# Optimization experiments

Hardware: AMD Instinct MI355X
Metric: run time of the kernel (lower is better)

## Reference

```python
import jax, jax.numpy as jnp
import numpy as np

D_MODEL = 1024
N_HEADS = 16
HEAD_DIM = D_MODEL // N_HEADS
BATCH = 4
SEQ = 2048
NEG_INF = -1000000000.0  # matches torch masked_fill value in source


def setup_inputs() -> dict:
    key = jax.random.key(0)
    ks = jax.random.split(key, 5)
    scale = 1.0 / np.sqrt(D_MODEL)
    x = jax.random.normal(ks[0], (BATCH, SEQ, D_MODEL), dtype=jnp.float32)
    wq = jax.random.normal(ks[1], (D_MODEL, D_MODEL), dtype=jnp.float32) * scale
    wk = jax.random.normal(ks[2], (D_MODEL, D_MODEL), dtype=jnp.float32) * scale
    wv = jax.random.normal(ks[3], (D_MODEL, D_MODEL), dtype=jnp.float32) * scale
    wo = jax.random.normal(ks[4], (D_MODEL, D_MODEL), dtype=jnp.float32) * scale
    return {"x": x, "wq": wq, "wk": wk, "wv": wv, "wo": wo}


def reference(x, wq, wk, wv, wo):
    b, s, d = x.shape
    # projections (weights applied as x @ W^T, matching nn-style Linear weights)
    q = jnp.einsum('bsd,ed->bse', x, wq).reshape(b, s, N_HEADS, HEAD_DIM).transpose(0, 2, 1, 3)
    k = jnp.einsum('bsd,ed->bse', x, wk).reshape(b, s, N_HEADS, HEAD_DIM).transpose(0, 2, 1, 3)
    v = jnp.einsum('bsd,ed->bse', x, wv).reshape(b, s, N_HEADS, HEAD_DIM).transpose(0, 2, 1, 3)
    # scaled dot-product scores [b, h, s, s]
    scores = jnp.einsum('bhqd,bhkd->bhqk', q, k) / jnp.sqrt(jnp.float32(HEAD_DIM))
    # causal mask: positions strictly above diagonal masked with -1e9
    causal = jnp.triu(jnp.ones((s, s), dtype=bool), k=1)
    scores = jnp.where(causal[None, None], jnp.float32(NEG_INF), scores)
    attn = jax.nn.softmax(scores, axis=-1)
    out = jnp.einsum('bhqk,bhkd->bhqd', attn, v)
    out = out.transpose(0, 2, 1, 3).reshape(b, s, d)
    return jnp.einsum('bsd,ed->bse', out, wo)
```

## Files before the change

kernel.cpp:

```cpp
#include <hip/hip_runtime.h>
#include <hip/hip_bf16.h>

typedef __hip_bfloat16 bf16;
typedef __attribute__((ext_vector_type(8))) short short8;
typedef __attribute__((ext_vector_type(4))) short short4_t;
typedef __attribute__((ext_vector_type(4))) float f32x4;
typedef unsigned int u32;

#define MFMA16(a, b, c) __builtin_amdgcn_mfma_f32_16x16x32_bf16(a, b, c, 0, 0, 0)

#if __has_builtin(__builtin_amdgcn_exp2f)
#define EXP2(x) __builtin_amdgcn_exp2f(x)
#else
#define EXP2(x) __expf((x) * 0.6931471805599453f)
#endif

static constexpr int S_ = 2048, D_ = 1024, M_ = 8192;
static constexpr size_t SZ = (size_t)M_ * D_;
static constexpr size_t WSZ = (size_t)D_ * D_;
static constexpr float QSCALE = 0.125f * 1.4426950408889634f;

__device__ __forceinline__ void gload16(void* lds, const void* g) {
  __builtin_amdgcn_global_load_lds((const __attribute__((address_space(1))) void*)g,
                                   (__attribute__((address_space(3))) void*)lds, 16, 0, 0);
}

__device__ __forceinline__ short4_t cvt4(const float4 v) {
  short4_t r;
  r[0] = (short)__bfloat16_as_ushort(__float2bfloat16(v.x));
  r[1] = (short)__bfloat16_as_ushort(__float2bfloat16(v.y));
  r[2] = (short)__bfloat16_as_ushort(__float2bfloat16(v.z));
  r[3] = (short)__bfloat16_as_ushort(__float2bfloat16(v.w));
  return r;
}

__device__ __forceinline__ u32 pk2(float a, float b) {
  return (u32)__bfloat16_as_ushort(__float2bfloat16(a)) |
         ((u32)__bfloat16_as_ushort(__float2bfloat16(b)) << 16);
}

__global__ __launch_bounds__(256) void cvt_f32_bf16(const float* __restrict__ in,
                                                    bf16* __restrict__ out, int n4) {
  int stride = gridDim.x * 256;
  for (int i = blockIdx.x * 256 + threadIdx.x; i < n4; i += stride) {
    float4 v = ((const float4*)in)[i];
    *(short4_t*)&out[(size_t)i * 4] = cvt4(v);
  }
}

__global__ __launch_bounds__(256) void cvt_all(const float* __restrict__ x,
                                               const float* __restrict__ wq,
                                               const float* __restrict__ wk,
                                               const float* __restrict__ wv,
                                               const float* __restrict__ wo,
                                               bf16* __restrict__ xb,
                                               bf16* __restrict__ wqkv,
                                               bf16* __restrict__ wob, int nseg) {
  const int X4 = (int)(SZ / 4);
  const int per = 1 << 18;
  int total = X4 + nseg * per;
  for (int i = blockIdx.x * 256 + threadIdx.x; i < total; i += gridDim.x * 256) {
    const float* s;
    bf16* d;
    int off;
    if (i < X4) {
      s = x; d = xb; off = i;
    } else {
      int j = i - X4;
      int seg = j >> 18;
      off = j & (per - 1);
      s = (seg == 0) ? wq : (seg == 1) ? wk : (seg == 2) ? wv : wo;
      d = (seg < 3) ? (wqkv + ((size_t)seg << 20)) : wob;
    }
    float4 v = ((const float4*)s)[off];
    *(short4_t*)&d[(size_t)off * 4] = cvt4(v);
  }
}

#define GSTAGE(buf, kt)                                                              \
  {                                                                                  \
    _Pragma("unroll") for (int i_ = 0; i_ < 2; ++i_) {                               \
      int c_ = i_ * 256 + tid;                                                       \
      int row_ = c_ >> 2, col_ = (c_ & 3) * 8;                                       \
      gload16(&lA[buf][c_ * 8], &A[(size_t)(m0 + row_) * 1024 + (kt) * 32 + col_]);  \
      gload16(&lB[buf][c_ * 8], &W[(size_t)(n0 + row_) * 1024 + (kt) * 32 + col_]);  \
    }                                                                                \
  }

__global__ __launch_bounds__(256) void qkv_gemm(const bf16* __restrict__ A,
                                                const bf16* __restrict__ Wqkv,
                                                bf16* __restrict__ QKV) {
  __shared__ __align__(16) bf16 lA[2][128 * 32];
  __shared__ __align__(16) bf16 lB[2][128 * 32];
  const int tid = threadIdx.x, lane = tid & 63, w = tid >> 6;
  const int wr = w >> 1, wc = w & 1;
  const int m0 = blockIdx.x * 128;
  const int mat = blockIdx.y >> 3, n0 = (blockIdx.y & 7) * 128;
  const bf16* W = Wqkv + (size_t)mat * WSZ;
  bf16* C = QKV + (size_t)mat * SZ;
  const int l15 = lane & 15, lg = lane >> 4;

  f32x4 zero = {0.f, 0.f, 0.f, 0.f};
  f32x4 acc[4][4];
#pragma unroll
  for (int i = 0; i < 4; i++)
#pragma unroll
    for (int j = 0; j < 4; j++) acc[i][j] = zero;

  GSTAGE(0, 0);
  int cur = 0;
  for (int kt = 0; kt < 32; ++kt) {
    if (kt + 1 < 32) {
      GSTAGE(cur ^ 1, kt + 1);
      asm volatile("s_waitcnt vmcnt(4)" ::: "memory");
    } else {
      asm volatile("s_waitcnt vmcnt(0)" ::: "memory");
    }
    __builtin_amdgcn_s_barrier();

    short8 af[4], bfr[4];
#pragma unroll
    for (int mi = 0; mi < 4; mi++)
      af[mi] = *(const short8*)&lA[cur][(wr * 64 + mi * 16 + l15) * 32 + lg * 8];
#pragma unroll
    for (int ni = 0; ni < 4; ni++)
      bfr[ni] = *(const short8*)&lB[cur][(wc * 64 + ni * 16 + l15) * 32 + lg * 8];
    if (mat == 2) {
#pragma unroll
      for (int mi = 0; mi < 4; mi++)
#pragma unroll
        for (int ni = 0; ni < 4; ni++) acc[mi][ni] = MFMA16(af[mi], bfr[ni], acc[mi][ni]);
    } else {
#pragma unroll
      for (int mi = 0; mi < 4; mi++)
#pragma unroll
        for (int ni = 0; ni < 4; ni++) acc[mi][ni] = MFMA16(bfr[ni], af[mi], acc[mi][ni]);
    }
    __builtin_amdgcn_s_barrier();
    cur ^= 1;
  }

  if (mat == 2) {
#pragma unroll
    for (int mi = 0; mi < 4; mi++)
#pragma unroll
      for (int ni = 0; ni < 4; ni++) {
        int mB = m0 + wr * 64 + mi * 16 + lg * 4;
        int n = n0 + wc * 64 + ni * 16 + l15;
        int b = mB >> 11, s = mB & 2047, h = n >> 6, dh = n & 63;
        uint2 dd = {pk2(acc[mi][ni][0], acc[mi][ni][1]),
                    pk2(acc[mi][ni][2], acc[mi][ni][3])};
        *(uint2*)&C[((size_t)((b << 4) + h) * 64 + dh) * 2048 + s] = dd;
      }
  } else {
    const float scale = (mat == 0) ? QSCALE : 1.0f;
#pragma unroll
    for (int mi = 0; mi < 4; mi++)
#pragma unroll
      for (int ni = 0; ni < 4; ni++) {
        int m = m0 + wr * 64 + mi * 16 + l15;
        int nB = n0 + wc * 64 + ni * 16 + lg * 4;
        int b = m >> 11, s = m & 2047, h = nB >> 6, dh = nB & 63;
        uint2 dd = {pk2(acc[mi][ni][0] * scale, acc[mi][ni][1] * scale),
                    pk2(acc[mi][ni][2] * scale, acc[mi][ni][3] * scale)};
        *(uint2*)&C[((size_t)((b << 4) + h) * 2048 + s) * 64 + dh] = dd;
      }
  }
}

__global__ __launch_bounds__(256) void gemm_out(const bf16* __restrict__ A,
                                                const bf16* __restrict__ W,
                                                float* __restrict__ C) {
  __shared__ __align__(16) bf16 lA[2][128 * 32];
  __shared__ __align__(16) bf16 lB[2][128 * 32];
  const int tid = threadIdx.x, lane = tid & 63, w = tid >> 6;
  const int wr = w >> 1, wc = w & 1;
  const int m0 = blockIdx.x * 128, n0 = blockIdx.y * 128;
  const int l15 = lane & 15, lg = lane >> 4;

  f32x4 zero = {0.f, 0.f, 0.f, 0.f};
  f32x4 acc[4][4];
#pragma unroll
  for (int i = 0; i < 4; i++)
#pragma unroll
    for (int j = 0; j < 4; j++) acc[i][j] = zero;

  GSTAGE(0, 0);
  int cur = 0;
  for (int kt = 0; kt < 32; ++kt) {
    if (kt + 1 < 32) {
      GSTAGE(cur ^ 1, kt + 1);
      asm volatile("s_waitcnt vmcnt(4)" ::: "memory");
    } else {
      asm volatile("s_waitcnt vmcnt(0)" ::: "memory");
    }
    __builtin_amdgcn_s_barrier();

    short8 af[4], bfr[4];
#pragma unroll
    for (int mi = 0; mi < 4; mi++)
      af[mi] = *(const short8*)&lA[cur][(wr * 64 + mi * 16 + l15) * 32 + lg * 8];
#pragma unroll
    for (int ni = 0; ni < 4; ni++)
      bfr[ni] = *(const short8*)&lB[cur][(wc * 64 + ni * 16 + l15) * 32 + lg * 8];
#pragma unroll
    for (int mi = 0; mi < 4; mi++)
#pragma unroll
      for (int ni = 0; ni < 4; ni++) acc[mi][ni] = MFMA16(bfr[ni], af[mi], acc[mi][ni]);
    __builtin_amdgcn_s_barrier();
    cur ^= 1;
  }

#pragma unroll
  for (int mi = 0; mi < 4; mi++)
#pragma unroll
    for (int ni = 0; ni < 4; ni++) {
      int m = m0 + wr * 64 + mi * 16 + l15;
      int nB = n0 + wc * 64 + ni * 16 + lg * 4;
      float4 v = {acc[mi][ni][0], acc[mi][ni][1], acc[mi][ni][2], acc[mi][ni][3]};
      *(float4*)&C[(size_t)m * 1024 + nB] = v;
    }
}

__global__ __launch_bounds__(256, 3) void attn_fwd(const bf16* __restrict__ Q,
                                                   const bf16* __restrict__ K,
                                                   const bf16* __restrict__ Vt,
                                                   bf16* __restrict__ O) {
  __shared__ __align__(16) bf16 lK[2][64 * 64];
  __shared__ __align__(16) bf16 lV[2][64 * 64];
  __shared__ __align__(16) bf16 lP[4][32 * 64];
  const int tid = threadIdx.x, lane = tid & 63, w = tid >> 6;
  const int l15 = lane & 15, lg = lane >> 4;
  const int bh = blockIdx.x;
  const int qb = 15 - blockIdx.y;
  const int q0 = qb * 128 + w * 32;
  const bf16* Qb = Q + (size_t)bh * S_ * 64;
  const bf16* Kb = K + (size_t)bh * S_ * 64;
  const bf16* Vb = Vt + (size_t)bh * 64 * S_;
  bf16* Pw = lP[w];

  short8 qf[2][2];
#pragma unroll
  for (int mi = 0; mi < 2; mi++)
#pragma unroll
    for (int kd = 0; kd < 2; kd++)
      qf[mi][kd] = *(const short8*)&Qb[(size_t)(q0 + mi * 16 + l15) * 64 + kd * 32 + lg * 8];

  f32x4 zero = {0.f, 0.f, 0.f, 0.f};
  f32x4 acc[2][4];
  float mr[2], lr[2];
#pragma unroll
  for (int mi = 0; mi < 2; mi++) {
    mr[mi] = -1e9f;
    lr[mi] = 0.f;
#pragma unroll
    for (int ni = 0; ni < 4; ni++) acc[mi][ni] = zero;
  }

  const int nch = (qb + 1) * 2;

#define STAGE(buf, c)                                                                   \
  {                                                                                     \
    _Pragma("unroll") for (int i = 0; i < 2; ++i) {                                     \
      int t2 = i * 256 + tid;                                                           \
      int row = t2 >> 3;                                                                \
      int cb = ((t2 & 7) * 16) ^ ((row & 7) << 4);                                      \
      gload16((char*)lK[buf] + t2 * 16, (const char*)Kb + (size_t)((c) * 64 + row) * 128 + cb); \
      gload16((char*)lV[buf] + t2 * 16, (const char*)Vb + (size_t)row * 4096 + (size_t)(c) * 128 + cb); \
    }                                                                                   \
  }

  STAGE(0, 0);
  int cur = 0;
  for (int c = 0; c < nch; ++c) {
    __builtin_amdgcn_s_barrier();
    if (c + 1 < nch) {
      STAGE(cur ^ 1, c + 1);
      asm volatile("s_waitcnt vmcnt(4)" ::: "memory");
    } else {
      asm volatile("s_waitcnt vmcnt(0)" ::: "memory");
    }
    __builtin_amdgcn_s_barrier();

    if (c * 64 <= q0 + 31) {
      const int c0 = c * 64;
      f32x4 sc[2][4];
#pragma unroll
      for (int mi = 0; mi < 2; mi++)
#pragma unroll
        for (int ch = 0; ch < 4; ch++) sc[mi][ch] = zero;
      const char* Kc = (const char*)lK[cur];
      __builtin_amdgcn_s_setprio(1);
#pragma unroll
      for (int kd = 0; kd < 2; ++kd)
#pragma unroll
        for (int ch = 0; ch < 4; ++ch) {
          short8 kf = *(const short8*)(Kc + (ch * 16 + l15) * 128 + ((kd * 64 + lg * 16) ^ ((l15 & 7) << 4)));
          sc[0][ch] = MFMA16(kf, qf[0][kd], sc[0][ch]);
          sc[1][ch] = MFMA16(kf, qf[1][kd], sc[1][ch]);
        }
      __builtin_amdgcn_s_setprio(0);

      if (c0 + 63 > q0) {
#pragma unroll
        for (int mi = 0; mi < 2; mi++) {
          int q = q0 + mi * 16 + l15;
#pragma unroll
          for (int ch = 0; ch < 4; ch++)
#pragma unroll
            for (int r = 0; r < 4; r++) {
              int kv = c0 + ch * 16 + lg * 4 + r;
              if (kv > q) sc[mi][ch][r] = -1e9f;
            }
        }
      }

#pragma unroll
      for (int mi = 0; mi < 2; mi++) {
        float v0 = fmaxf(fmaxf(sc[mi][0][0], sc[mi][0][1]), fmaxf(sc[mi][0][2], sc[mi][0][3]));
        float v1 = fmaxf(fmaxf(sc[mi][1][0], sc[mi][1][1]), fmaxf(sc[mi][1][2], sc[mi][1][3]));
        float v2 = fmaxf(fmaxf(sc[mi][2][0], sc[mi][2][1]), fmaxf(sc[mi][2][2], sc[mi][2][3]));
        float v3 = fmaxf(fmaxf(sc[mi][3][0], sc[mi][3][1]), fmaxf(sc[mi][3][2], sc[mi][3][3]));
        float vmax = fmaxf(fmaxf(v0, v1), fmaxf(v2, v3));
        vmax = fmaxf(vmax, __shfl_xor(vmax, 16));
        vmax = fmaxf(vmax, __shfl_xor(vmax, 32));
        if (!__all(vmax <= mr[mi] + 8.f)) {
          float mn = fmaxf(mr[mi], vmax);
          float corr = EXP2(mr[mi] - mn);
          mr[mi] = mn;
          lr[mi] *= corr;
#pragma unroll
          for (int r = 0; r < 4; r++) {
            float cr = __shfl(corr, (lane & 48) | (((lane >> 4) << 2) + r));
#pragma unroll
            for (int ni = 0; ni < 4; ni++) acc[mi][ni][r] *= cr;
          }
        }
        float ps0 = 0.f, ps1 = 0.f, ps2 = 0.f, ps3 = 0.f;
#pragma unroll
        for (int ch = 0; ch < 4; ch++) {
          float p0 = EXP2(sc[mi][ch][0] - mr[mi]);
          float p1 = EXP2(sc[mi][ch][1] - mr[mi]);
          float p2 = EXP2(sc[mi][ch][2] - mr[mi]);
          float p3 = EXP2(sc[mi][ch][3] - mr[mi]);
          sc[mi][ch][0] = p0; sc[mi][ch][1] = p1; sc[mi][ch][2] = p2; sc[mi][ch][3] = p3;
          ps0 += p0; ps1 += p1; ps2 += p2; ps3 += p3;
        }
        float ps = (ps0 + ps1) + (ps2 + ps3);
        ps += __shfl_xor(ps, 16);
        ps += __shfl_xor(ps, 32);
        lr[mi] += ps;
        int row = mi * 16 + l15;
        char* Pb = (char*)Pw + row * 128;
        int sw = (row & 7) << 4;
#pragma unroll
        for (int ch = 0; ch < 4; ch++) {
          u32 d0 = pk2(sc[mi][ch][0], sc[mi][ch][1]);
          u32 d1 = pk2(sc[mi][ch][2], sc[mi][ch][3]);
          uint2 dd = {d0, d1};
          *(uint2*)(Pb + ((ch * 32 + lg * 8) ^ sw)) = dd;
        }
      }

      asm volatile("s_waitcnt lgkmcnt(0)" ::: "memory");
      const char* Vc = (const char*)lV[cur];
      __builtin_amdgcn_s_setprio(1);
#pragma unroll
      for (int kd = 0; kd < 2; ++kd) {
        short8 pf[2];
#pragma unroll
        for (int mi = 0; mi < 2; mi++)
          pf[mi] = *(const short8*)((const char*)Pw + (mi * 16 + l15) * 128 +
                                    ((kd * 64 + lg * 16) ^ ((l15 & 7) << 4)));
#pragma unroll
        for (int ni = 0; ni < 4; ++ni) {
          short8 vf = *(const short8*)(Vc + (ni * 16 + l15) * 128 + ((kd * 64 + lg * 16) ^ ((l15 & 7) << 4)));
          acc[0][ni] = MFMA16(pf[0], vf, acc[0][ni]);
          acc[1][ni] = MFMA16(pf[1], vf, acc[1][ni]);
        }
      }
      __builtin_amdgcn_s_setprio(0);
    }
    cur ^= 1;
  }
#undef STAGE

  const int b = bh >> 4, h = bh & 15;
#pragma unroll
  for (int mi = 0; mi < 2; mi++) {
    float lrr[4];
#pragma unroll
    for (int r = 0; r < 4; r++)
      lrr[r] = __shfl(lr[mi], (lane & 48) | (((lane >> 4) << 2) + r));
#pragma unroll
    for (int ni = 0; ni < 4; ni++)
#pragma unroll
      for (int r = 0; r < 4; r++) {
        int q = q0 + mi * 16 + lg * 4 + r;
        size_t idx = ((size_t)(b * 2048 + q)) * 1024 + h * 64 + ni * 16 + l15;
        O[idx] = __float2bfloat16(acc[mi][ni][r] / lrr[r]);
      }
  }
}

extern "C" void kernel_launch(void* const* d_in, const int* in_sizes, int n_in,
                              void* d_out, int out_size, void* d_ws, size_t ws_size,
                              hipStream_t stream) {
  const float* x = (const float*)d_in[0];
  const float* wq = (const float*)d_in[1];
  const float* wk = (const float*)d_in[2];
  const float* wv = (const float*)d_in[3];
  const float* wo = (const float*)d_in[4];
  float* out = (float*)d_out;

  bf16* xb = (bf16*)d_ws;
  bf16* Qw = xb + SZ;
  bf16* AO = xb;
  bf16* wqkv = (bf16*)d_out;

  const bool ws_has_wo = ws_size >= (4 * SZ + WSZ) * sizeof(bf16);
  bf16* wob = ws_has_wo ? (xb + 4 * SZ) : Qw;

  dim3 blk(256);
  hipLaunchKernelGGL(cvt_all, dim3(2048), blk, 0, stream, x, wq, wk, wv, wo, xb, wqkv, wob,
                     ws_has_wo ? 4 : 3);
  hipLaunchKernelGGL(qkv_gemm, dim3(64, 24), blk, 0, stream, xb, wqkv, Qw);
  hipLaunchKernelGGL(attn_fwd, dim3(64, 16), blk, 0, stream, Qw, Qw + SZ, Qw + 2 * SZ, AO);
  if (!ws_has_wo)
    hipLaunchKernelGGL(cvt_f32_bf16, dim3(512), blk, 0, stream, wo, wob, (int)(WSZ / 4));
  hipLaunchKernelGGL(gemm_out, dim3(64, 8), blk, 0, stream, AO, wob, out);
}
```

Baseline: 279.1 us.

## Unroll double-buffered loops by two with static buffers and one barrier per step

The QKV GEMM, output GEMM and attention loops are unrolled by two so each half uses a compile-time LDS buffer index. Each half issues the next tile's async global-to-LDS load, computes on the other buffer, then hits a single __syncthreads. This replaces the hand-placed vmcnt waits and two s_barriers per iteration. The aim is less barrier and address overhead and better scheduling, at the cost of larger code and __syncthreads' full waitcnt semantics, which could reduce overlap.

```diff
diff --git a/kernel.cpp b/kernel.cpp
--- a/kernel.cpp
+++ b/kernel.cpp
@@ -77,14 +77,38 @@
   }
 }
 
-#define GSTAGE(buf, kt)                                                              \
-  {                                                                                  \
-    _Pragma("unroll") for (int i_ = 0; i_ < 2; ++i_) {                               \
-      int c_ = i_ * 256 + tid;                                                       \
-      int row_ = c_ >> 2, col_ = (c_ & 3) * 8;                                       \
-      gload16(&lA[buf][c_ * 8], &A[(size_t)(m0 + row_) * 1024 + (kt) * 32 + col_]);  \
-      gload16(&lB[buf][c_ * 8], &W[(size_t)(n0 + row_) * 1024 + (kt) * 32 + col_]);  \
-    }                                                                                \
+#define GSTAGE(b, kt)                                                                 \
+  {                                                                                   \
+    _Pragma("unroll") for (int i_ = 0; i_ < 2; ++i_) {                                \
+      int c_ = i_ * 256 + tid;                                                        \
+      int row_ = c_ >> 2, col_ = (c_ & 3) * 8;                                        \
+      gload16(&lA[b][c_ * 8], &A[(size_t)(m0 + row_) * 1024 + (kt) * 32 + col_]);     \
+      gload16(&lB[b][c_ * 8], &W[(size_t)(n0 + row_) * 1024 + (kt) * 32 + col_]);     \
+    }                                                                                 \
+  }
+
+#define GCOMP_SWAP(b)                                                                 \
+  {                                                                                   \
+    short8 af[4], bfr[4];                                                             \
+    _Pragma("unroll") for (int mi = 0; mi < 4; mi++)                                  \
+        af[mi] = *(const short8*)&lA[b][(wr * 64 + mi * 16 + l15) * 32 + lg * 8];     \
+    _Pragma("unroll") for (int ni = 0; ni < 4; ni++)                                  \
+        bfr[ni] = *(const short8*)&lB[b][(wc * 64 + ni * 16 + l15) * 32 + lg * 8];    \
+    _Pragma("unroll") for (int mi = 0; mi < 4; mi++)                                  \
+        _Pragma("unroll") for (int ni = 0; ni < 4; ni++)                              \
+            acc[mi][ni] = MFMA16(bfr[ni], af[mi], acc[mi][ni]);                       \
+  }
+
+#define GCOMP_NORM(b)                                                                 \
+  {                                                                                   \
+    short8 af[4], bfr[4];                                                             \
+    _Pragma("unroll") for (int mi = 0; mi < 4; mi++)                                  \
+        af[mi] = *(const short8*)&lA[b][(wr * 64 + mi * 16 + l15) * 32 + lg * 8];     \
+    _Pragma("unroll") for (int ni = 0; ni < 4; ni++)                                  \
+        bfr[ni] = *(const short8*)&lB[b][(wc * 64 + ni * 16 + l15) * 32 + lg * 8];    \
+    _Pragma("unroll") for (int mi = 0; mi < 4; mi++)                                  \
+        _Pragma("unroll") for (int ni = 0; ni < 4; ni++)                              \
+            acc[mi][ni] = MFMA16(af[mi], bfr[ni], acc[mi][ni]);                       \
   }
 
 __global__ __launch_bounds__(256) void qkv_gemm(const bf16* __restrict__ A,
@@ -108,36 +132,14 @@
     for (int j = 0; j < 4; j++) acc[i][j] = zero;
 
   GSTAGE(0, 0);
-  int cur = 0;
-  for (int kt = 0; kt < 32; ++kt) {
-    if (kt + 1 < 32) {
-      GSTAGE(cur ^ 1, kt + 1);
-      asm volatile("s_waitcnt vmcnt(4)" ::: "memory");
-    } else {
-      asm volatile("s_waitcnt vmcnt(0)" ::: "memory");
-    }
-    __builtin_amdgcn_s_barrier();
-
-    short8 af[4], bfr[4];
-#pragma unroll
-    for (int mi = 0; mi < 4; mi++)
-      af[mi] = *(const short8*)&lA[cur][(wr * 64 + mi * 16 + l15) * 32 + lg * 8];
-#pragma unroll
-    for (int ni = 0; ni < 4; ni++)
-      bfr[ni] = *(const short8*)&lB[cur][(wc * 64 + ni * 16 + l15) * 32 + lg * 8];
-    if (mat == 2) {
-#pragma unroll
-      for (int mi = 0; mi < 4; mi++)
-#pragma unroll
-        for (int ni = 0; ni < 4; ni++) acc[mi][ni] = MFMA16(af[mi], bfr[ni], acc[mi][ni]);
-    } else {
-#pragma unroll
-      for (int mi = 0; mi < 4; mi++)
-#pragma unroll
-        for (int ni = 0; ni < 4; ni++) acc[mi][ni] = MFMA16(bfr[ni], af[mi], acc[mi][ni]);
-    }
-    __builtin_amdgcn_s_barrier();
-    cur ^= 1;
+  __syncthreads();
+  for (int kt = 0; kt < 32; kt += 2) {
+    GSTAGE(1, kt + 1);
+    if (mat == 2) GCOMP_NORM(0) else GCOMP_SWAP(0);
+    __syncthreads();
+    if (kt + 2 < 32) GSTAGE(0, kt + 2);
+    if (mat == 2) GCOMP_NORM(1) else GCOMP_SWAP(1);
+    __syncthreads();
   }
 
   if (mat == 2) {
@@ -186,29 +188,14 @@
     for (int j = 0; j < 4; j++) acc[i][j] = zero;
 
   GSTAGE(0, 0);
-  int cur = 0;
-  for (int kt = 0; kt < 32; ++kt) {
-    if (kt + 1 < 32) {
-      GSTAGE(cur ^ 1, kt + 1);
-      asm volatile("s_waitcnt vmcnt(4)" ::: "memory");
-    } else {
-      asm volatile("s_waitcnt vmcnt(0)" ::: "memory");
-    }
-    __builtin_amdgcn_s_barrier();
-
-    short8 af[4], bfr[4];
-#pragma unroll
-    for (int mi = 0; mi < 4; mi++)
-      af[mi] = *(const short8*)&lA[cur][(wr * 64 + mi * 16 + l15) * 32 + lg * 8];
-#pragma unroll
-    for (int ni = 0; ni < 4; ni++)
-      bfr[ni] = *(const short8*)&lB[cur][(wc * 64 + ni * 16 + l15) * 32 + lg * 8];
-#pragma unroll
-    for (int mi = 0; mi < 4; mi++)
-#pragma unroll
-      for (int ni = 0; ni < 4; ni++) acc[mi][ni] = MFMA16(bfr[ni], af[mi], acc[mi][ni]);
-    __builtin_amdgcn_s_barrier();
-    cur ^= 1;
+  __syncthreads();
+  for (int kt = 0; kt < 32; kt += 2) {
+    GSTAGE(1, kt + 1);
+    GCOMP_SWAP(0);
+    __syncthreads();
+    if (kt + 2 < 32) GSTAGE(0, kt + 2);
+    GCOMP_SWAP(1);
+    __syncthreads();
   }
 
 #pragma unroll
@@ -270,120 +257,103 @@
     }                                                                                   \
   }
 
+#define ATTN_CHUNK(CC, BUF)                                                             \
+  if ((CC) * 64 <= q0 + 31) {                                                           \
+    const int c0 = (CC) * 64;                                                           \
+    const char* Kc = (const char*)lK[BUF];                                              \
+    const char* Vc = (const char*)lV[BUF];                                              \
+    f32x4 sc[2][4];                                                                     \
+    _Pragma("unroll") for (int mi = 0; mi < 2; mi++)                                    \
+        _Pragma("unroll") for (int ch = 0; ch < 4; ch++) sc[mi][ch] = zero;             \
+    __builtin_amdgcn_s_setprio(1);                                                      \
+    _Pragma("unroll") for (int kd = 0; kd < 2; ++kd)                                    \
+        _Pragma("unroll") for (int ch = 0; ch < 4; ++ch) {                              \
+      short8 kf = *(const short8*)(Kc + (ch * 16 + l15) * 128 +                         \
+                                   ((kd * 64 + lg * 16) ^ ((l15 & 7) << 4)));           \
+      sc[0][ch] = MFMA16(kf, qf[0][kd], sc[0][ch]);                                     \
+      sc[1][ch] = MFMA16(kf, qf[1][kd], sc[1][ch]);                                     \
+    }                                                                                   \
+    __builtin_amdgcn_s_setprio(0);                                                      \
+    if (c0 + 63 > q0) {                                                                 \
+      _Pragma("unroll") for (int mi = 0; mi < 2; mi++) {                                \
+        int q = q0 + mi * 16 + l15;                                                     \
+        _Pragma("unroll") for (int ch = 0; ch < 4; ch++)                                \
+            _Pragma("unroll") for (int r = 0; r < 4; r++) {                             \
+          int kv = c0 + ch * 16 + lg * 4 + r;                                           \
+          if (kv > q) sc[mi][ch][r] = -1e9f;                                            \
+        }                                                                               \
+      }                                                                                 \
+    }                                                                                   \
+    _Pragma("unroll") for (int mi = 0; mi < 2; mi++) {                                  \
+      float v0 = fmaxf(fmaxf(sc[mi][0][0], sc[mi][0][1]), fmaxf(sc[mi][0][2], sc[mi][0][3])); \
+      float v1 = fmaxf(fmaxf(sc[mi][1][0], sc[mi][1][1]), fmaxf(sc[mi][1][2], sc[mi][1][3])); \
+      float v2 = fmaxf(fmaxf(sc[mi][2][0], sc[mi][2][1]), fmaxf(sc[mi][2][2], sc[mi][2][3])); \
+      float v3 = fmaxf(fmaxf(sc[mi][3][0], sc[mi][3][1]), fmaxf(sc[mi][3][2], sc[mi][3][3])); \
+      float vmax = fmaxf(fmaxf(v0, v1), fmaxf(v2, v3));                                 \
+      vmax = fmaxf(vmax, __shfl_xor(vmax, 16));                                         \
+      vmax = fmaxf(vmax, __shfl_xor(vmax, 32));                                         \
+      if (!__all(vmax <= mr[mi] + 8.f)) {                                               \
+        float mn = fmaxf(mr[mi], vmax);                                                 \
+        float corr = EXP2(mr[mi] - mn);                                                 \
+        mr[mi] = mn;                                                                    \
+        lr[mi] *= corr;                                                                 \
+        _Pragma("unroll") for (int r = 0; r < 4; r++) {                                 \
+          float cr = __shfl(corr, (lane & 48) | (((lane >> 4) << 2) + r));              \
+          _Pragma("unroll") for (int ni = 0; ni < 4; ni++) acc[mi][ni][r] *= cr;        \
+        }                                                                               \
+      }                                                                                 \
+      float ps0 = 0.f, ps1 = 0.f, ps2 = 0.f, ps3 = 0.f;                                 \
+      _Pragma("unroll") for (int ch = 0; ch < 4; ch++) {                                \
+        float p0 = EXP2(sc[mi][ch][0] - mr[mi]);                                        \
+        float p1 = EXP2(sc[mi][ch][1] - mr[mi]);                                        \
+        float p2 = EXP2(sc[mi][ch][2] - mr[mi]);                                        \
+        float p3 = EXP2(sc[mi][ch][3] - mr[mi]);                                        \
+        sc[mi][ch][0] = p0; sc[mi][ch][1] = p1; sc[mi][ch][2] = p2; sc[mi][ch][3] = p3; \
+        ps0 += p0; ps1 += p1; ps2 += p2; ps3 += p3;                                     \
+      }                                                                                 \
+      float ps = (ps0 + ps1) + (ps2 + ps3);                                             \
+      ps += __shfl_xor(ps, 16);                                                         \
+      ps += __shfl_xor(ps, 32);                                                         \
+      lr[mi] += ps;                                                                     \
+      int row = mi * 16 + l15;                                                          \
+      char* Pb = (char*)Pw + row * 128;                                                 \
+      int sw = (row & 7) << 4;                                                          \
+      _Pragma("unroll") for (int ch = 0; ch < 4; ch++) {                                \
+        u32 d0 = pk2(sc[mi][ch][0], sc[mi][ch][1]);                                     \
+        u32 d1 = pk2(sc[mi][ch][2], sc[mi][ch][3]);                                     \
+        uint2 dd = {d0, d1};                                                            \
+        *(uint2*)(Pb + ((ch * 32 + lg * 8) ^ sw)) = dd;                                 \
+      }                                                                                 \
+    }                                                                                   \
+    asm volatile("s_waitcnt lgkmcnt(0)" ::: "memory");                                  \
+    __builtin_amdgcn_s_setprio(1);                                                      \
+    _Pragma("unroll") for (int kd = 0; kd < 2; ++kd) {                                  \
+      short8 pf[2];                                                                     \
+      _Pragma("unroll") for (int mi = 0; mi < 2; mi++)                                  \
+          pf[mi] = *(const short8*)((const char*)Pw + (mi * 16 + l15) * 128 +           \
+                                    ((kd * 64 + lg * 16) ^ ((l15 & 7) << 4)));          \
+      _Pragma("unroll") for (int ni = 0; ni < 4; ++ni) {                                \
+        short8 vf = *(const short8*)(Vc + (ni * 16 + l15) * 128 +                       \
+                                     ((kd * 64 + lg * 16) ^ ((l15 & 7) << 4)));         \
+        acc[0][ni] = MFMA16(pf[0], vf, acc[0][ni]);                                     \
+        acc[1][ni] = MFMA16(pf[1], vf, acc[1][ni]);                                     \
+      }                                                                                 \
+    }                                                                                   \
+    __builtin_amdgcn_s_setprio(0);                                                      \
+  }
+
   STAGE(0, 0);
-  int cur = 0;
-  for (int c = 0; c < nch; ++c) {
-    __builtin_amdgcn_s_barrier();
-    if (c + 1 < nch) {
-      STAGE(cur ^ 1, c + 1);
-      asm volatile("s_waitcnt vmcnt(4)" ::: "memory");
-    } else {
-      asm volatile("s_waitcnt vmcnt(0)" ::: "memory");
-    }
-    __builtin_amdgcn_s_barrier();
-
-    if (c * 64 <= q0 + 31) {
-      const int c0 = c * 64;
-      f32x4 sc[2][4];
-#pragma unroll
-      for (int mi = 0; mi < 2; mi++)
-#pragma unroll
-        for (int ch = 0; ch < 4; ch++) sc[mi][ch] = zero;
-      const char* Kc = (const char*)lK[cur];
-      __builtin_amdgcn_s_setprio(1);
-#pragma unroll
-      for (int kd = 0; kd < 2; ++kd)
-#pragma unroll
-        for (int ch = 0; ch < 4; ++ch) {
-          short8 kf = *(const short8*)(Kc + (ch * 16 + l15) * 128 + ((kd * 64 + lg * 16) ^ ((l15 & 7) << 4)));
-          sc[0][ch] = MFMA16(kf, qf[0][kd], sc[0][ch]);
-          sc[1][ch] = MFMA16(kf, qf[1][kd], sc[1][ch]);
-        }
-      __builtin_amdgcn_s_setprio(0);
-
-      if (c0 + 63 > q0) {
-#pragma unroll
-        for (int mi = 0; mi < 2; mi++) {
-          int q = q0 + mi * 16 + l15;
-#pragma unroll
-          for (int ch = 0; ch < 4; ch++)
-#pragma unroll
-            for (int r = 0; r < 4; r++) {
-              int kv = c0 + ch * 16 + lg * 4 + r;
-              if (kv > q) sc[mi][ch][r] = -1e9f;
-            }
-        }
-      }
-
-#pragma unroll
-      for (int mi = 0; mi < 2; mi++) {
-        float v0 = fmaxf(fmaxf(sc[mi][0][0], sc[mi][0][1]), fmaxf(sc[mi][0][2], sc[mi][0][3]));
-        float v1 = fmaxf(fmaxf(sc[mi][1][0], sc[mi][1][1]), fmaxf(sc[mi][1][2], sc[mi][1][3]));
-        float v2 = fmaxf(fmaxf(sc[mi][2][0], sc[mi][2][1]), fmaxf(sc[mi][2][2], sc[mi][2][3]));
-        float v3 = fmaxf(fmaxf(sc[mi][3][0], sc[mi][3][1]), fmaxf(sc[mi][3][2], sc[mi][3][3]));
-        float vmax = fmaxf(fmaxf(v0, v1), fmaxf(v2, v3));
-        vmax = fmaxf(vmax, __shfl_xor(vmax, 16));
-        vmax = fmaxf(vmax, __shfl_xor(vmax, 32));
-        if (!__all(vmax <= mr[mi] + 8.f)) {
-          float mn = fmaxf(mr[mi], vmax);
-          float corr = EXP2(mr[mi] - mn);
-          mr[mi] = mn;
-          lr[mi] *= corr;
-#pragma unroll
-          for (int r = 0; r < 4; r++) {
-            float cr = __shfl(corr, (lane & 48) | (((lane >> 4) << 2) + r));
-#pragma unroll
-            for (int ni = 0; ni < 4; ni++) acc[mi][ni][r] *= cr;
-          }
-        }
-        float ps0 = 0.f, ps1 = 0.f, ps2 = 0.f, ps3 = 0.f;
-#pragma unroll
-        for (int ch = 0; ch < 4; ch++) {
-          float p0 = EXP2(sc[mi][ch][0] - mr[mi]);
-          float p1 = EXP2(sc[mi][ch][1] - mr[mi]);
-          float p2 = EXP2(sc[mi][ch][2] - mr[mi]);
-          float p3 = EXP2(sc[mi][ch][3] - mr[mi]);
-          sc[mi][ch][0] = p0; sc[mi][ch][1] = p1; sc[mi][ch][2] = p2; sc[mi][ch][3] = p3;
-          ps0 += p0; ps1 += p1; ps2 += p2; ps3 += p3;
-        }
-        float ps = (ps0 + ps1) + (ps2 + ps3);
-        ps += __shfl_xor(ps, 16);
-        ps += __shfl_xor(ps, 32);
-        lr[mi] += ps;
-        int row = mi * 16 + l15;
-        char* Pb = (char*)Pw + row * 128;
-        int sw = (row & 7) << 4;
-#pragma unroll
-        for (int ch = 0; ch < 4; ch++) {
-          u32 d0 = pk2(sc[mi][ch][0], sc[mi][ch][1]);
-          u32 d1 = pk2(sc[mi][ch][2], sc[mi][ch][3]);
-          uint2 dd = {d0, d1};
-          *(uint2*)(Pb + ((ch * 32 + lg * 8) ^ sw)) = dd;
-        }
-      }
-
-      asm volatile("s_waitcnt lgkmcnt(0)" ::: "memory");
-      const char* Vc = (const char*)lV[cur];
-      __builtin_amdgcn_s_setprio(1);
-#pragma unroll
-      for (int kd = 0; kd < 2; ++kd) {
-        short8 pf[2];
-#pragma unroll
-        for (int mi = 0; mi < 2; mi++)
-          pf[mi] = *(const short8*)((const char*)Pw + (mi * 16 + l15) * 128 +
-                                    ((kd * 64 + lg * 16) ^ ((l15 & 7) << 4)));
-#pragma unroll
-        for (int ni = 0; ni < 4; ++ni) {
-          short8 vf = *(const short8*)(Vc + (ni * 16 + l15) * 128 + ((kd * 64 + lg * 16) ^ ((l15 & 7) << 4)));
-          acc[0][ni] = MFMA16(pf[0], vf, acc[0][ni]);
-          acc[1][ni] = MFMA16(pf[1], vf, acc[1][ni]);
-        }
-      }
-      __builtin_amdgcn_s_setprio(0);
-    }
-    cur ^= 1;
+  __syncthreads();
+  for (int c = 0; c < nch; c += 2) {
+    STAGE(1, c + 1);
+    ATTN_CHUNK(c, 0);
+    __syncthreads();
+    if (c + 2 < nch) STAGE(0, c + 2);
+    ATTN_CHUNK(c + 1, 1);
+    __syncthreads();
   }
 #undef STAGE
+#undef ATTN_CHUNK
 
   const int b = bh >> 4, h = bh & 15;
 #pragma unroll
```

Result: faster. 262.3 us (-6.0%).
